# Optimization experiments

Hardware: AMD Instinct MI355X
Metric: run time of the kernel (lower is better)

Reference implementation:

```python
import jax, jax.numpy as jnp
import numpy as np

N = 8192
IN_DIM = 512
OUT_DIM = 256
ALPHA = 0.2  # LeakyReLU negative slope


def setup_inputs() -> dict:
    key = jax.random.key(0)
    k_nodes, k_edge, k_W, k_Wb, k_a1, k_a1b, k_a2, k_a2b = jax.random.split(key, 8)
    nodes = jax.random.normal(k_nodes, (N, IN_DIM), dtype=jnp.float32)
    edge_mat = jax.random.uniform(k_edge, (N, N)) > 0.5
    edge_mat = edge_mat | jnp.eye(N, dtype=bool)
    s_W = 1.0 / np.sqrt(IN_DIM)
    s_a = 1.0 / np.sqrt(OUT_DIM)
    W_w = jax.random.uniform(k_W, (OUT_DIM, IN_DIM), minval=-s_W, maxval=s_W, dtype=jnp.float32)
    W_b = jax.random.uniform(k_Wb, (OUT_DIM,), minval=-s_W, maxval=s_W, dtype=jnp.float32)
    a1_w = jax.random.uniform(k_a1, (1, OUT_DIM), minval=-s_a, maxval=s_a, dtype=jnp.float32)
    a1_b = jax.random.uniform(k_a1b, (1,), minval=-s_a, maxval=s_a, dtype=jnp.float32)
    a2_w = jax.random.uniform(k_a2, (1, OUT_DIM), minval=-s_a, maxval=s_a, dtype=jnp.float32)
    a2_b = jax.random.uniform(k_a2b, (1,), minval=-s_a, maxval=s_a, dtype=jnp.float32)
    return {"nodes": nodes, "edge_mat": edge_mat, "W_w": W_w, "W_b": W_b,
            "a1_w": a1_w, "a1_b": a1_b, "a2_w": a2_w, "a2_b": a2_b}


def reference(nodes, edge_mat, W_w, W_b, a1_w, a1_b, a2_w, a2_b):
    Wh = nodes @ W_w.T + W_b                      # [N, OUT_DIM]
    Wh1 = Wh @ a1_w.T + a1_b                      # [N, 1]
    Wh2 = Wh @ a2_w.T + a2_b                      # [N, 1]
    scores = jax.nn.leaky_relu(Wh1 + Wh2.T, negative_slope=ALPHA)  # [N, N]
    masked = jnp.where(edge_mat, scores, -jnp.inf)
    attention = jax.nn.softmax(masked, axis=1)    # [N, N]
    return attention @ Wh                         # [N, OUT_DIM]
```

## Files before the change

### kernel.cpp

```cpp
#include <hip/hip_runtime.h>
#include <hip/hip_bf16.h>
#include <stdint.h>


#define NN 8192
#define IND 512
#define OUTD 256

typedef __attribute__((ext_vector_type(8))) short short8;
typedef __attribute__((ext_vector_type(4))) short short4v;
typedef __attribute__((ext_vector_type(4))) float f32x4;

#define AS_GLOBAL __attribute__((address_space(1)))
#define AS_LDS __attribute__((address_space(3)))

static __device__ __forceinline__ short f2bf(float f) {
  return __builtin_bit_cast(short, __float2bfloat16(f));
}

extern "C" __global__ __launch_bounds__(256) void k_convert_w(
    const float* __restrict__ W, short* __restrict__ W2) {
  const int t = blockIdx.x * 256 + threadIdx.x;
  const int row = t >> 6, kb = t & 63;
  const float* src = W + row * IND + kb * 8;
  f32x4 x0 = *(const f32x4*)src;
  f32x4 x1 = *(const f32x4*)(src + 4);
  short8 o;
  o[0] = f2bf(x0[0]); o[1] = f2bf(x0[1]); o[2] = f2bf(x0[2]); o[3] = f2bf(x0[3]);
  o[4] = f2bf(x1[0]); o[5] = f2bf(x1[1]); o[6] = f2bf(x1[2]); o[7] = f2bf(x1[3]);
  *(short8*)(W2 + (size_t)kb * 2048 + row * 8) = o;
}

extern "C" __global__ __launch_bounds__(128) void k_wh(
    const float* __restrict__ nodes, const short* __restrict__ W2,
    const float* __restrict__ Wb, const float* __restrict__ a1w,
    const float* __restrict__ a1b, const float* __restrict__ a2w,
    const float* __restrict__ a2b, short* __restrict__ WhL,
    float* __restrict__ s1, float* __restrict__ s2) {
  const int tid = threadIdx.x;
  const int wv = tid >> 6, lane = tid & 63, g = lane >> 4, m = lane & 15;
  const int rowbase = blockIdx.x * 32 + wv * 16;

  f32x4 acc[16];
#pragma unroll
  for (int nf = 0; nf < 16; ++nf) acc[nf] = (f32x4){0.f, 0.f, 0.f, 0.f};

  const float* arow = nodes + (size_t)(rowbase + m) * IND;
  const short* bb = W2 + (size_t)g * 2048 + m * 8;
#pragma unroll 4
  for (int k0 = 0; k0 < IND; k0 += 32) {
    const float* ap = arow + k0 + g * 8;
    f32x4 x0 = *(const f32x4*)ap;
    f32x4 x1 = *(const f32x4*)(ap + 4);
    short8 af;
    af[0] = f2bf(x0[0]); af[1] = f2bf(x0[1]); af[2] = f2bf(x0[2]); af[3] = f2bf(x0[3]);
    af[4] = f2bf(x1[0]); af[5] = f2bf(x1[1]); af[6] = f2bf(x1[2]); af[7] = f2bf(x1[3]);
    const short* bk = bb + (size_t)(k0 >> 3) * 2048;
#pragma unroll
    for (int nf = 0; nf < 16; ++nf) {
      short8 bf = *(const short8*)(bk + nf * 128);
      acc[nf] = __builtin_amdgcn_mfma_f32_16x16x32_bf16(af, bf, acc[nf], 0, 0, 0);
    }
  }

  float p1[4] = {0.f, 0.f, 0.f, 0.f}, p2[4] = {0.f, 0.f, 0.f, 0.f};
#pragma unroll
  for (int nf = 0; nf < 16; ++nf) {
    const int n = nf * 16 + m;
    const float b = Wb[n], c1 = a1w[n], c2 = a2w[n];
#pragma unroll
    for (int r = 0; r < 4; ++r) {
      float v = acc[nf][r] + b;
      acc[nf][r] = v;
      p1[r] += c1 * v;
      p2[r] += c2 * v;
    }
  }
#pragma unroll
  for (int off = 1; off < 16; off <<= 1) {
#pragma unroll
    for (int r = 0; r < 4; ++r) {
      p1[r] += __shfl_xor(p1[r], off);
      p2[r] += __shfl_xor(p2[r], off);
    }
  }
  if (m == 0) {
    const float b1 = a1b[0], b2 = a2b[0];
#pragma unroll
    for (int r = 0; r < 4; ++r) {
      const int row = rowbase + g * 4 + r;
      s1[row] = p1[r] + b1;
      s2[row] = p2[r] + b2;
    }
  }

  const size_t cbase = ((size_t)(rowbase >> 3) + (g >> 1)) * 2048 + (g & 1) * 4;
#pragma unroll
  for (int nf = 0; nf < 16; ++nf) {
    short4v o;
#pragma unroll
    for (int r = 0; r < 4; ++r) o[r] = f2bf(acc[nf][r]);
    *(short4v*)(WhL + cbase + (size_t)(nf * 16 + m) * 8) = o;
  }
}

extern "C" __global__ __launch_bounds__(256) void k_mask(
    const int* __restrict__ mask, uint32_t* __restrict__ bm) {
  const int tid = threadIdx.x;
  const int wv = tid >> 6, lane = tid & 63;
  const int gw = blockIdx.x * 4 + wv;
  const size_t base = (size_t)gw * 16384;
#pragma unroll 4
  for (int it = 0; it < 64; ++it) {
    const size_t ib = base + (size_t)it * 256;
    unsigned long long b0 = __ballot(mask[ib + lane] != 0);
    unsigned long long b1 = __ballot(mask[ib + 64 + lane] != 0);
    unsigned long long b2 = __ballot(mask[ib + 128 + lane] != 0);
    unsigned long long b3 = __ballot(mask[ib + 192 + lane] != 0);
    if (lane < 8) {
      unsigned long long s01 = (lane & 2) ? b1 : b0;
      unsigned long long s23 = (lane & 2) ? b3 : b2;
      unsigned long long sel = (lane & 4) ? s23 : s01;
      bm[ib / 32 + lane] = (uint32_t)(sel >> ((lane & 1) * 32));
    }
  }
}

extern "C" __global__ __launch_bounds__(256, 4) void k_attn(
    const uint32_t* __restrict__ bm, const short* __restrict__ WhL,
    const float* __restrict__ s1, const float* __restrict__ s2,
    float* __restrict__ pnum, float* __restrict__ pden) {
  __shared__ short Bs[2][8192];

  const int tid = threadIdx.x;
  const int w = tid >> 6, lane = tid & 63, g = lane >> 4, m = lane & 15;
  const int rt = blockIdx.x >> 3, jc = blockIdx.x & 7;
  const int rg = w & 1, ns = w >> 1;
  const int rb = rt * 64 + rg * 32;

  const float s1a = s1[rb + m];
  const float s1b = s1[rb + 16 + m];

  f32x4 acc0[8], acc1[8];
#pragma unroll
  for (int nf = 0; nf < 8; ++nf) {
    acc0[nf] = (f32x4){0.f, 0.f, 0.f, 0.f};
    acc1[nf] = (f32x4){0.f, 0.f, 0.f, 0.f};
  }
  float den0 = 0.f, den1 = 0.f;

  const uint32_t* bw0 = bm + (size_t)(rb + m) * 256 + jc * 32;
  const uint32_t* bw1 = bw0 + (size_t)16 * 256;
  const float* sp = s2 + jc * 1024 + g * 8;
  const short* gWu = WhL + (size_t)jc * 262144 + w * 2048 + lane * 8;

  auto build = [&](float s1h, uint32_t bits, const f32x4& slo, const f32x4& shi,
                   float& den) -> short8 {
    short8 af;
#pragma unroll
    for (int i = 0; i < 8; ++i) {
      float sv = s1h + (i < 4 ? slo[i] : shi[i - 4]);
      sv = fmaxf(sv, 0.2f * sv);
      float pv = (bits & (1u << i)) ? __expf(sv) : 0.f;
      den += pv;
      af[i] = f2bf(pv);
    }
    return af;
  };

#pragma unroll
  for (int c = 0; c < 4; ++c) {
    __builtin_amdgcn_global_load_lds(
        (const AS_GLOBAL void*)(gWu + c * 512),
        (AS_LDS void*)(&Bs[0][w * 2048 + c * 512]), 16, 0, 0);
  }
  uint32_t cw0 = bw0[0], cw1 = bw1[0];
  __syncthreads();

  for (int u = 0; u < 32; ++u) {
    if (u < 31) {
      const short* gn = gWu + (size_t)(u + 1) * 8192;
      short* ld = &Bs[(u + 1) & 1][w * 2048];
#pragma unroll
      for (int c = 0; c < 4; ++c) {
        __builtin_amdgcn_global_load_lds(
            (const AS_GLOBAL void*)(gn + c * 512),
            (AS_LDS void*)(ld + c * 512), 16, 0, 0);
      }
    }
    const int un = (u < 31) ? u + 1 : 31;
    const uint32_t nw0 = bw0[un], nw1 = bw1[un];

    const f32x4 cs0 = *(const f32x4*)(sp + u * 32);
    const f32x4 cs1 = *(const f32x4*)(sp + u * 32 + 4);
    short8 af0 = build(s1a, cw0 >> (g * 8), cs0, cs1, den0);
    short8 af1 = build(s1b, cw1 >> (g * 8), cs0, cs1, den1);
    const short* bl = &Bs[u & 1][g * 2048 + (ns * 128 + m) * 8];
#pragma unroll
    for (int nf = 0; nf < 8; ++nf) {
      short8 bf = *(const short8*)(bl + nf * 128);
      acc0[nf] = __builtin_amdgcn_mfma_f32_16x16x32_bf16(af0, bf, acc0[nf], 0, 0, 0);
      acc1[nf] = __builtin_amdgcn_mfma_f32_16x16x32_bf16(af1, bf, acc1[nf], 0, 0, 0);
    }
    cw0 = nw0; cw1 = nw1;
    __syncthreads();
  }

  den0 += __shfl_xor(den0, 16); den0 += __shfl_xor(den0, 32);
  den1 += __shfl_xor(den1, 16); den1 += __shfl_xor(den1, 32);
  if (ns == 0 && lane < 16) {
    pden[jc * NN + rb + m] = den0;
    pden[jc * NN + rb + 16 + m] = den1;
  }

  float* pn = pnum + (size_t)jc * NN * OUTD + (size_t)rb * OUTD + ns * 128;
#pragma unroll
  for (int r = 0; r < 4; ++r) {
    const int q = g * 4 + r;
#pragma unroll
    for (int nf = 0; nf < 8; ++nf) {
      pn[(size_t)q * OUTD + nf * 16 + m] = acc0[nf][r];
      pn[(size_t)(16 + q) * OUTD + nf * 16 + m] = acc1[nf][r];
    }
  }
}

extern "C" __global__ __launch_bounds__(256) void k_comb(
    const float* __restrict__ pnum, const float* __restrict__ pden,
    float* __restrict__ out) {
  const int idx = blockIdx.x * 256 + threadIdx.x;
  const int row = idx >> 6, c4 = (idx & 63) * 4;
  f32x4 s = (f32x4){0.f, 0.f, 0.f, 0.f};
  float d = 0.f;
#pragma unroll
  for (int jc = 0; jc < 8; ++jc) {
    f32x4 v = *(const f32x4*)(pnum + ((size_t)jc * NN + row) * OUTD + c4);
    s += v;
    d += pden[jc * NN + row];
  }
  const float inv = 1.f / d;
  *(f32x4*)(out + (size_t)row * OUTD + c4) = s * inv;
}

extern "C" void kernel_launch(void* const* d_in, const int* in_sizes, int n_in,
                              void* d_out, int out_size, void* d_ws, size_t ws_size,
                              hipStream_t stream) {
  const float* nodes = (const float*)d_in[0];
  const int*   mask  = (const int*)d_in[1];
  const float* W_w   = (const float*)d_in[2];
  const float* W_b   = (const float*)d_in[3];
  const float* a1w   = (const float*)d_in[4];
  const float* a1b   = (const float*)d_in[5];
  const float* a2w   = (const float*)d_in[6];
  const float* a2b   = (const float*)d_in[7];
  float* out = (float*)d_out;

  char* ws = (char*)d_ws;
  short*    WhL  = (short*)(ws);
  float*    s1   = (float*)(ws + (size_t)4  * 1024 * 1024);
  float*    s2   = (float*)(ws + (size_t)4  * 1024 * 1024 + 32768);
  short*    W2   = (short*)(ws + (size_t)4  * 1024 * 1024 + 65536);
  uint32_t* bmp  = (uint32_t*)(ws + (size_t)5  * 1024 * 1024);
  float*    pnum = (float*)(ws + (size_t)16 * 1024 * 1024);
  float*    pden = (float*)(ws + (size_t)96 * 1024 * 1024);

  hipLaunchKernelGGL(k_convert_w, dim3(64), dim3(256), 0, stream, W_w, W2);
  hipLaunchKernelGGL(k_wh, dim3(256), dim3(128), 0, stream,
                     nodes, W2, W_b, a1w, a1b, a2w, a2b, WhL, s1, s2);
  hipLaunchKernelGGL(k_mask, dim3(1024), dim3(256), 0, stream, mask, bmp);
  hipLaunchKernelGGL(k_attn, dim3(1024), dim3(256), 0, stream,
                     bmp, WhL, s1, s2, pnum, pden);
  hipLaunchKernelGGL(k_comb, dim3(2048), dim3(256), 0, stream,
                     pnum, pden, out);
}
```

Before: 185.5 us.

## Factor exp of leaky-ReLU scores into precomputed per-node exponentials

Precomputes exp(s1), exp(0.2*s1), exp(s2), exp(0.2*s2) in a new prep kernel and packs the s2 terms with a bf16 copy of s2 into a buffer staged into LDS. The attention kernel then builds each weight with a sign test and one multiply instead of an expf per score pair, cutting transcendental VALU work in the hot loop. The sign test uses a bf16-rounded s2, so near-zero sums may pick the other branch, and products of exponentials could overflow for large scores. The mask kernel launch is also moved earlier.

```diff
diff --git a/kernel.cpp b/kernel.cpp
--- a/kernel.cpp
+++ b/kernel.cpp
@@ -10,6 +10,7 @@
 typedef __attribute__((ext_vector_type(8))) short short8;
 typedef __attribute__((ext_vector_type(4))) short short4v;
 typedef __attribute__((ext_vector_type(4))) float f32x4;
+typedef __attribute__((ext_vector_type(4))) unsigned int u32x4;
 
 #define AS_GLOBAL __attribute__((address_space(1)))
 #define AS_LDS __attribute__((address_space(3)))
@@ -102,6 +103,19 @@
     for (int r = 0; r < 4; ++r) o[r] = f2bf(acc[nf][r]);
     *(short4v*)(WhL + cbase + (size_t)(nf * 16 + m) * 8) = o;
   }
+}
+
+extern "C" __global__ __launch_bounds__(256) void k_prep(
+    const float* __restrict__ s1, const float* __restrict__ s2,
+    float* __restrict__ sAC, uint32_t* __restrict__ sPK) {
+  const int i = blockIdx.x * 256 + threadIdx.x;
+  const float v1 = s1[i], v2 = s2[i];
+  sAC[i] = __expf(v1);
+  sAC[NN + i] = __expf(0.2f * v1);
+  const float B = __expf(v2), D = __expf(0.2f * v2);
+  sPK[2 * i] = __builtin_bit_cast(uint32_t, B);
+  sPK[2 * i + 1] =
+      ((uint32_t)(uint16_t)f2bf(D) << 16) | (uint16_t)(uint16_t)f2bf(v2);
 }
 
 extern "C" __global__ __launch_bounds__(256) void k_mask(
@@ -128,9 +142,11 @@
 
 extern "C" __global__ __launch_bounds__(256, 4) void k_attn(
     const uint32_t* __restrict__ bm, const short* __restrict__ WhL,
-    const float* __restrict__ s1, const float* __restrict__ s2,
+    const float* __restrict__ s1, const float* __restrict__ sAC,
+    const uint32_t* __restrict__ sPK,
     float* __restrict__ pnum, float* __restrict__ pden) {
   __shared__ short Bs[2][8192];
+  __shared__ uint32_t PKs[2048];
 
   const int tid = threadIdx.x;
   const int w = tid >> 6, lane = tid & 63, g = lane >> 4, m = lane & 15;
@@ -138,8 +154,9 @@
   const int rg = w & 1, ns = w >> 1;
   const int rb = rt * 64 + rg * 32;
 
-  const float s1a = s1[rb + m];
-  const float s1b = s1[rb + 16 + m];
+  const float T0 = -s1[rb + m],        T1 = -s1[rb + 16 + m];
+  const float A0 = sAC[rb + m],        A1 = sAC[rb + 16 + m];
+  const float C0 = sAC[NN + rb + m],   C1 = sAC[NN + rb + 16 + m];
 
   f32x4 acc0[8], acc1[8];
 #pragma unroll
@@ -151,23 +168,15 @@
 
   const uint32_t* bw0 = bm + (size_t)(rb + m) * 256 + jc * 32;
   const uint32_t* bw1 = bw0 + (size_t)16 * 256;
-  const float* sp = s2 + jc * 1024 + g * 8;
   const short* gWu = WhL + (size_t)jc * 262144 + w * 2048 + lane * 8;
 
-  auto build = [&](float s1h, uint32_t bits, const f32x4& slo, const f32x4& shi,
-                   float& den) -> short8 {
-    short8 af;
-#pragma unroll
-    for (int i = 0; i < 8; ++i) {
-      float sv = s1h + (i < 4 ? slo[i] : shi[i - 4]);
-      sv = fmaxf(sv, 0.2f * sv);
-      float pv = (bits & (1u << i)) ? __expf(sv) : 0.f;
-      den += pv;
-      af[i] = f2bf(pv);
-    }
-    return af;
-  };
-
+#pragma unroll
+  for (int c = 0; c < 2; ++c) {
+    __builtin_amdgcn_global_load_lds(
+        (const AS_GLOBAL void*)((const char*)sPK + (size_t)jc * 8192 +
+                                w * 2048 + c * 1024 + lane * 16),
+        (AS_LDS void*)((char*)PKs + w * 2048 + c * 1024), 16, 0, 0);
+  }
 #pragma unroll
   for (int c = 0; c < 4; ++c) {
     __builtin_amdgcn_global_load_lds(
@@ -176,6 +185,28 @@
   }
   uint32_t cw0 = bw0[0], cw1 = bw1[0];
   __syncthreads();
+
+  auto build = [&](float T, float A, float C, uint32_t mbits,
+                   const u32x4& q0, const u32x4& q1,
+                   const u32x4& q2, const u32x4& q3, float& den) -> short8 {
+    const uint32_t Bv[8] = {q0[0], q0[2], q1[0], q1[2],
+                            q2[0], q2[2], q3[0], q3[2]};
+    const uint32_t Dv[8] = {q0[1], q0[3], q1[1], q1[3],
+                            q2[1], q2[3], q3[1], q3[3]};
+    short8 af;
+#pragma unroll
+    for (int i = 0; i < 8; ++i) {
+      const float s2v = __builtin_bit_cast(float, Dv[i] << 16);
+      const bool pos = s2v > T;
+      const float wv = __builtin_bit_cast(float, pos ? Bv[i] : (Dv[i] & 0xFFFF0000u));
+      const float a = pos ? A : C;
+      const float val = wv * a;
+      const float pv = ((mbits >> i) & 1u) ? val : 0.f;
+      den += pv;
+      af[i] = f2bf(pv);
+    }
+    return af;
+  };
 
   for (int u = 0; u < 32; ++u) {
     if (u < 31) {
@@ -191,10 +222,13 @@
     const int un = (u < 31) ? u + 1 : 31;
     const uint32_t nw0 = bw0[un], nw1 = bw1[un];
 
-    const f32x4 cs0 = *(const f32x4*)(sp + u * 32);
-    const f32x4 cs1 = *(const f32x4*)(sp + u * 32 + 4);
-    short8 af0 = build(s1a, cw0 >> (g * 8), cs0, cs1, den0);
-    short8 af1 = build(s1b, cw1 >> (g * 8), cs0, cs1, den1);
+    const uint32_t* pk = &PKs[(u * 32 + g * 8) * 2];
+    const u32x4 q0 = *(const u32x4*)(pk + 0);
+    const u32x4 q1 = *(const u32x4*)(pk + 4);
+    const u32x4 q2 = *(const u32x4*)(pk + 8);
+    const u32x4 q3 = *(const u32x4*)(pk + 12);
+    short8 af0 = build(T0, A0, C0, cw0 >> (g * 8), q0, q1, q2, q3, den0);
+    short8 af1 = build(T1, A1, C1, cw1 >> (g * 8), q0, q1, q2, q3, den1);
     const short* bl = &Bs[u & 1][g * 2048 + (ns * 128 + m) * 8];
 #pragma unroll
     for (int nf = 0; nf < 8; ++nf) {
@@ -261,15 +295,18 @@
   float*    s2   = (float*)(ws + (size_t)4  * 1024 * 1024 + 32768);
   short*    W2   = (short*)(ws + (size_t)4  * 1024 * 1024 + 65536);
   uint32_t* bmp  = (uint32_t*)(ws + (size_t)5  * 1024 * 1024);
+  float*    sAC  = (float*)(ws + (size_t)13 * 1024 * 1024);
+  uint32_t* sPK  = (uint32_t*)(ws + (size_t)14 * 1024 * 1024);
   float*    pnum = (float*)(ws + (size_t)16 * 1024 * 1024);
   float*    pden = (float*)(ws + (size_t)96 * 1024 * 1024);
 
+  hipLaunchKernelGGL(k_mask, dim3(1024), dim3(256), 0, stream, mask, bmp);
   hipLaunchKernelGGL(k_convert_w, dim3(64), dim3(256), 0, stream, W_w, W2);
   hipLaunchKernelGGL(k_wh, dim3(256), dim3(128), 0, stream,
                      nodes, W2, W_b, a1w, a1b, a2w, a2b, WhL, s1, s2);
-  hipLaunchKernelGGL(k_mask, dim3(1024), dim3(256), 0, stream, mask, bmp);
+  hipLaunchKernelGGL(k_prep, dim3(32), dim3(256), 0, stream, s1, s2, sAC, sPK);
   hipLaunchKernelGGL(k_attn, dim3(1024), dim3(256), 0, stream,
-                     bmp, WhL, s1, s2, pnum, pden);
+                     bmp, WhL, s1, sAC, sPK, pnum, pden);
   hipLaunchKernelGGL(k_comb, dim3(2048), dim3(256), 0, stream,
                      pnum, pden, out);
 }
```

Measured after the change: 177.8 us. 1.04x faster.
